# Optimization experiments

Hardware: AMD Instinct MI355X
Metric: run time of the kernel (lower is better)

Reference implementation:

```python
import jax, jax.numpy as jnp
import numpy as np

B, T = 256, 512          # sequences, timesteps (batched over pyro.markov loop)
DATA_DIM = 88            # piano-roll tones
HIDDEN_DIM = 16          # HMM latent states
NN_DIM = 48
NN_CHANNELS = 2
KERNEL = 3


def _uniform(key, shape, fan_in):
    bound = 1.0 / np.sqrt(fan_in)
    return jax.random.uniform(key, shape, minval=-bound, maxval=bound, dtype=jnp.float32)


def setup_inputs() -> dict:
    key = jax.random.key(0)
    ks = jax.random.split(key, 13)
    w = jax.random.randint(ks[0], (B, T, 1), 0, HIDDEN_DIM)
    x = jax.random.randint(ks[1], (B, T, 1), 0, HIDDEN_DIM)
    y = jax.random.uniform(ks[2], (B, T, DATA_DIM), dtype=jnp.float32)
    return {
        "w": w, "x": x, "y": y,
        # nn.Linear(hidden_dim, nn_dim) for x and w one-hots
        "W_xh": _uniform(ks[3], (NN_DIM, HIDDEN_DIM), HIDDEN_DIM),
        "b_xh": _uniform(ks[4], (NN_DIM,), HIDDEN_DIM),
        "W_wh": _uniform(ks[5], (NN_DIM, HIDDEN_DIM), HIDDEN_DIM),
        "b_wh": _uniform(ks[6], (NN_DIM,), HIDDEN_DIM),
        # nn.Linear(nn_channels*data_dim, nn_dim)
        "W_yh": _uniform(ks[7], (NN_DIM, NN_CHANNELS * DATA_DIM), NN_CHANNELS * DATA_DIM),
        "b_yh": _uniform(ks[8], (NN_DIM,), NN_CHANNELS * DATA_DIM),
        # nn.Conv1d(1, nn_channels, 3, padding=1)
        "W_conv": _uniform(ks[9], (NN_CHANNELS, 1, KERNEL), KERNEL),
        "b_conv": _uniform(ks[10], (NN_CHANNELS,), KERNEL),
        # nn.Linear(nn_dim, data_dim)
        "W_hl": _uniform(ks[11], (DATA_DIM, NN_DIM), NN_DIM),
        "b_hl": _uniform(ks[12], (DATA_DIM,), NN_DIM),
    }


def _tones_generator(w, x, y, W_xh, b_xh, W_wh, b_wh, W_yh, b_yh, W_conv, b_conv, W_hl, b_hl):
    b, t, d = y.shape
    # one-hot scatter of the latent state indices (trailing index dim of size 1)
    w_onehot = jax.nn.one_hot(w[..., 0], HIDDEN_DIM, dtype=y.dtype)   # [B,T,H]
    x_onehot = jax.nn.one_hot(x[..., 0], HIDDEN_DIM, dtype=y.dtype)   # [B,T,H]
    # Conv1d(1 -> nn_channels, k=3, pad=1) over the tone axis
    y_nch = y.reshape(b * t, 1, d)                                    # [BT,1,D]
    y_conv = jax.lax.conv_general_dilated(
        y_nch, W_conv, window_strides=(1,), padding=[(1, 1)],
        dimension_numbers=("NCH", "OIH", "NCH"))
    y_conv = jax.nn.relu(y_conv + b_conv[None, :, None])              # [BT,C,D]
    y_conv = y_conv.reshape(b, t, NN_CHANNELS * d)                    # [B,T,C*D]
    h = jax.nn.relu(
        jnp.einsum("bth,nh->btn", x_onehot, W_xh) + b_xh
        + jnp.einsum("bth,nh->btn", w_onehot, W_wh) + b_wh
        + jnp.einsum("btc,nc->btn", y_conv, W_yh) + b_yh)             # [B,T,ND]
    return jnp.einsum("btn,dn->btd", h, W_hl) + b_hl                  # [B,T,D]


def reference(w, x, y, W_xh, b_xh, W_wh, b_wh, W_yh, b_yh, W_conv, b_conv, W_hl, b_hl):
    return _tones_generator(w, x, y, W_xh, b_xh, W_wh, b_wh, W_yh, b_yh,
                            W_conv, b_conv, W_hl, b_hl)
```

## Files before the change

kernel.cpp:

```cpp
#include <hip/hip_runtime.h>
#include <stdint.h>

#define NTOK (256 * 512)
#define TPB 256

typedef short bf16x8 __attribute__((ext_vector_type(8)));
typedef float f32x4 __attribute__((ext_vector_type(4)));
typedef unsigned short u16;
typedef unsigned int u32;

#define B1_U16 10752
#define B2_U16 6144
#define W_BYTES ((B1_U16 + B2_U16) * 2)
#define W_CHUNKS (W_BYTES / 16)
#define YB_U16 2816
#define H_U16 1024

__device__ __forceinline__ u16 f2bf(float f) {
    u32 u = __float_as_uint(f);
    return (u16)((u + 0x7fffu + ((u >> 16) & 1u)) >> 16);
}
__device__ __forceinline__ u32 cvtpk(float lo, float hi) {
    u32 r;
    asm("v_cvt_pk_bf16_f32 %0, %1, %2" : "=v"(r) : "v"(lo), "v"(hi));
    return r;
}
__device__ __forceinline__ void gll16(const void* g, void* l) {
    __builtin_amdgcn_global_load_lds(
        (const __attribute__((address_space(1))) void*)g,
        (__attribute__((address_space(3))) void*)l, 16, 0, 0);
}
__device__ __forceinline__ void gll4(const void* g, void* l) {
    __builtin_amdgcn_global_load_lds(
        (const __attribute__((address_space(1))) void*)g,
        (__attribute__((address_space(3))) void*)l, 4, 0, 0);
}

__global__ __launch_bounds__(256, 1)
void prep_weights(const float* __restrict__ Wxh, const float* __restrict__ bxh,
                  const float* __restrict__ Wwh, const float* __restrict__ bwh,
                  const float* __restrict__ Wyh, const float* __restrict__ byh,
                  const float* __restrict__ Whl, const float* __restrict__ bhl,
                  u16* __restrict__ ws)
{
    int e = blockIdx.x * 256 + threadIdx.x;
    if (e < B1_U16) {
        int j = e & 7, n = (e >> 3) % 48, kc = e / 384;
        int k = kc * 8 + j;
        float v;
        if (k < 176)       v = Wyh[n * 176 + (k & 1) * 88 + (k >> 1)];
        else if (k < 192)  v = Wxh[n * 16 + (k - 176)];
        else if (k < 208)  v = Wwh[n * 16 + (k - 192)];
        else if (k == 208) v = bxh[n] + bwh[n] + byh[n];
        else               v = 0.0f;
        ws[e] = f2bf(v);
    } else if (e < B1_U16 + B2_U16) {
        int e2 = e - B1_U16;
        int j = e2 & 7, dd = (e2 >> 3) % 96, kc = e2 / 768;
        int k = kc * 8 + j;
        float v = 0.0f;
        if (dd < 88) {
            if (k < 48)       v = Whl[dd * 48 + k];
            else if (k == 48) v = bhl[dd];
        }
        ws[e] = f2bf(v);
    }
}

__global__ __launch_bounds__(256, 2)
void tones_v8(const int* __restrict__ widx, const int* __restrict__ xidx,
              const float* __restrict__ y,
              const float* __restrict__ Wconv, const float* __restrict__ bconv,
              const u16* __restrict__ wsb,
              float* __restrict__ out)
{
    __shared__ __align__(16) u16 lds[32256];

    const int tid = threadIdx.x;
    const int wave = tid >> 6, lane = tid & 63;
    const int q = lane >> 4, c = lane & 15;

    const int tb = blockIdx.x * 64 + wave * 16;

    #pragma unroll
    for (int i = 0; i < 8; i++) {
        const int cb = i * 256 + wave * 64;
        gll16((const char*)wsb + (cb + lane) * 16, (char*)lds + cb * 16);
    }
    if (wave == 0) {
        const int cb = 2048;
        gll16((const char*)wsb + (cb + lane) * 16, (char*)lds + cb * 16);
    }

    u16* sYu = lds + 16896 + wave * YB_U16;
    {
        const char* yt = (const char*)(y + (size_t)tb * 88);
        char* dst = (char*)sYu;
        #pragma unroll
        for (int j = 0; j < 5; j++)
            gll16(yt + j * 1024 + lane * 16, dst + j * 1024);
        #pragma unroll
        for (int k = 0; k < 2; k++)
            gll4(yt + 5120 + k * 256 + lane * 4, dst + 5120 + k * 256);
    }

    const int xv = xidx[tb + c];
    const int wv = widx[tb + c];
    const float wc00 = Wconv[0], wc01 = Wconv[1], wc02 = Wconv[2];
    const float wc10 = Wconv[3], wc11 = Wconv[4], wc12 = Wconv[5];
    const float bc0 = bconv[0], bc1 = bconv[1];

    u16* sW = lds + 28160 + wave * H_U16;
    if (lane < 32) {
        uint4 hz = make_uint4((lane < 16) ? 0x3F80u : 0u, 0, 0, 0);
        *(uint4*)(sW + ((6 + (lane >> 4)) * 16 + (lane & 15)) * 8) = hz;
    }

    __syncthreads();

    const float* yr = (const float*)sYu + c * 88;

    f32x4 h0 = {0, 0, 0, 0}, h1 = {0, 0, 0, 0}, h2 = {0, 0, 0, 0};

    const u16* f1 = lds + (q * 48 + c) * 8;
    const u16* f2 = lds + B1_U16 + (q * 96 + c) * 8;

    #pragma unroll
    for (int ks = 0; ks < 7; ks++) {
        bf16x8 af;
        if (ks < 5) {
            const int d0 = 16 * ks + 4 * q;
            float p0 = (d0 == 0) ? 0.0f : yr[d0 - 1];
            f32x4 v4 = *(const f32x4*)(yr + d0);
            float p5 = yr[d0 + 4];
            float p[6] = {p0, v4[0], v4[1], v4[2], v4[3], p5};
            #pragma unroll
            for (int i = 0; i < 4; i++) {
                float c0 = fmaf(wc00, p[i], fmaf(wc01, p[i + 1], fmaf(wc02, p[i + 2], bc0)));
                float c1 = fmaf(wc10, p[i], fmaf(wc11, p[i + 1], fmaf(wc12, p[i + 2], bc1)));
                u32 pk = cvtpk(fmaxf(c0, 0.0f), fmaxf(c1, 0.0f));
                af[2 * i]     = (short)(pk & 0xFFFF);
                af[2 * i + 1] = (short)(pk >> 16);
            }
        } else if (ks == 5) {
            if (q < 2) {
                const int d0 = 80 + 4 * q;
                float p0 = yr[d0 - 1];
                f32x4 v4 = *(const f32x4*)(yr + d0);
                float p5 = (q == 0) ? yr[84] : 0.0f;
                float p[6] = {p0, v4[0], v4[1], v4[2], v4[3], p5};
                #pragma unroll
                for (int i = 0; i < 4; i++) {
                    float c0 = fmaf(wc00, p[i], fmaf(wc01, p[i + 1], fmaf(wc02, p[i + 2], bc0)));
                    float c1 = fmaf(wc10, p[i], fmaf(wc11, p[i + 1], fmaf(wc12, p[i + 2], bc1)));
                    u32 pk = cvtpk(fmaxf(c0, 0.0f), fmaxf(c1, 0.0f));
                    af[2 * i]     = (short)(pk & 0xFFFF);
                    af[2 * i + 1] = (short)(pk >> 16);
                }
            } else {
                const int base = (q - 2) * 8;
                #pragma unroll
                for (int j = 0; j < 8; j++)
                    af[j] = (short)((base + j == xv) ? 0x3F80 : 0);
            }
        } else {
            if (q < 2) {
                const int base = q * 8;
                #pragma unroll
                for (int j = 0; j < 8; j++)
                    af[j] = (short)((base + j == wv) ? 0x3F80 : 0);
            } else {
                #pragma unroll
                for (int j = 0; j < 8; j++)
                    af[j] = (short)((q == 2 && j == 0) ? 0x3F80 : 0);
            }
        }
        bf16x8 b0 = *(const bf16x8*)(f1 + (ks * 192 +  0) * 8);
        bf16x8 b1 = *(const bf16x8*)(f1 + (ks * 192 + 16) * 8);
        bf16x8 b2 = *(const bf16x8*)(f1 + (ks * 192 + 32) * 8);
        h0 = __builtin_amdgcn_mfma_f32_16x16x32_bf16(af, b0, h0, 0, 0, 0);
        h1 = __builtin_amdgcn_mfma_f32_16x16x32_bf16(af, b1, h1, 0, 0, 0);
        h2 = __builtin_amdgcn_mfma_f32_16x16x32_bf16(af, b2, h2, 0, 0, 0);
    }

    #pragma unroll
    for (int r = 0; r < 4; r++) {
        const int row = q * 4 + r;
        sW[((0 + (c >> 3)) * 16 + row) * 8 + (c & 7)] = (u16)cvtpk(fmaxf(h0[r], 0.0f), 0.0f);
        sW[((2 + (c >> 3)) * 16 + row) * 8 + (c & 7)] = (u16)cvtpk(fmaxf(h1[r], 0.0f), 0.0f);
        sW[((4 + (c >> 3)) * 16 + row) * 8 + (c & 7)] = (u16)cvtpk(fmaxf(h2[r], 0.0f), 0.0f);
    }

    f32x4 o0 = {0,0,0,0}, o1 = {0,0,0,0}, o2 = {0,0,0,0};
    f32x4 o3 = {0,0,0,0}, o4 = {0,0,0,0}, o5 = {0,0,0,0};
    #pragma unroll
    for (int ks = 0; ks < 2; ks++) {
        bf16x8 a2 = *(const bf16x8*)(sW + ((ks * 4 + q) * 16 + c) * 8);
        bf16x8 w0 = *(const bf16x8*)(f2 + (ks * 384 +  0) * 8);
        bf16x8 w1 = *(const bf16x8*)(f2 + (ks * 384 + 16) * 8);
        bf16x8 w2 = *(const bf16x8*)(f2 + (ks * 384 + 32) * 8);
        bf16x8 w3 = *(const bf16x8*)(f2 + (ks * 384 + 48) * 8);
        bf16x8 w4 = *(const bf16x8*)(f2 + (ks * 384 + 64) * 8);
        bf16x8 w5 = *(const bf16x8*)(f2 + (ks * 384 + 80) * 8);
        o0 = __builtin_amdgcn_mfma_f32_16x16x32_bf16(a2, w0, o0, 0, 0, 0);
        o1 = __builtin_amdgcn_mfma_f32_16x16x32_bf16(a2, w1, o1, 0, 0, 0);
        o2 = __builtin_amdgcn_mfma_f32_16x16x32_bf16(a2, w2, o2, 0, 0, 0);
        o3 = __builtin_amdgcn_mfma_f32_16x16x32_bf16(a2, w3, o3, 0, 0, 0);
        o4 = __builtin_amdgcn_mfma_f32_16x16x32_bf16(a2, w4, o4, 0, 0, 0);
        o5 = __builtin_amdgcn_mfma_f32_16x16x32_bf16(a2, w5, o5, 0, 0, 0);
    }

    float* orow = out + (size_t)(tb + q * 4) * 88;
    #pragma unroll
    for (int r = 0; r < 4; r++) {
        orow[r * 88 +  0 + c] = o0[r];
        orow[r * 88 + 16 + c] = o1[r];
        orow[r * 88 + 32 + c] = o2[r];
        orow[r * 88 + 48 + c] = o3[r];
        orow[r * 88 + 64 + c] = o4[r];
        if (c < 8) orow[r * 88 + 80 + c] = o5[r];
    }
}

extern "C" void kernel_launch(void* const* d_in, const int* in_sizes, int n_in,
                              void* d_out, int out_size, void* d_ws, size_t ws_size,
                              hipStream_t stream) {
    (void)in_sizes; (void)n_in; (void)out_size; (void)ws_size;
    u16* ws = (u16*)d_ws;
    prep_weights<<<dim3(66), dim3(TPB), 0, stream>>>(
        (const float*)d_in[3],  (const float*)d_in[4],
        (const float*)d_in[5],  (const float*)d_in[6],
        (const float*)d_in[7],  (const float*)d_in[8],
        (const float*)d_in[11], (const float*)d_in[12], ws);
    tones_v8<<<dim3(NTOK / 64), dim3(TPB), 0, stream>>>(
        (const int*)d_in[0], (const int*)d_in[1], (const float*)d_in[2],
        (const float*)d_in[9], (const float*)d_in[10], ws, (float*)d_out);
}
```

Baseline: 124.7 us.

## Overlap weight staging with conv compute and stage output through LDS

Issues the per-tile y loads first and the weight LDS loads after them, split into contiguous per-wave chunks. A partial vmcnt wait lets each wave compute all conv and one-hot A fragments from its y tile while the weight loads are still in flight, replacing the block-wide syncthreads with a later wait plus barrier. Outputs are written to the wave's LDS y buffer and then stored to global memory as coalesced 16-byte vectors instead of scattered 4-byte stores. This raises register pressure by holding seven A fragments, and it depends on exact vmcnt counting being correct.

```diff
diff --git a/kernel.cpp b/kernel.cpp
--- a/kernel.cpp
+++ b/kernel.cpp
@@ -11,8 +11,6 @@
 
 #define B1_U16 10752
 #define B2_U16 6144
-#define W_BYTES ((B1_U16 + B2_U16) * 2)
-#define W_CHUNKS (W_BYTES / 16)
 #define YB_U16 2816
 #define H_U16 1024
 
@@ -68,7 +66,7 @@
 }
 
 __global__ __launch_bounds__(256, 2)
-void tones_v8(const int* __restrict__ widx, const int* __restrict__ xidx,
+void tones_v9(const int* __restrict__ widx, const int* __restrict__ xidx,
               const float* __restrict__ y,
               const float* __restrict__ Wconv, const float* __restrict__ bconv,
               const u16* __restrict__ wsb,
@@ -82,15 +80,8 @@
 
     const int tb = blockIdx.x * 64 + wave * 16;
 
-    #pragma unroll
-    for (int i = 0; i < 8; i++) {
-        const int cb = i * 256 + wave * 64;
-        gll16((const char*)wsb + (cb + lane) * 16, (char*)lds + cb * 16);
-    }
-    if (wave == 0) {
-        const int cb = 2048;
-        gll16((const char*)wsb + (cb + lane) * 16, (char*)lds + cb * 16);
-    }
+    const int xv = xidx[tb + c];
+    const int wv = widx[tb + c];
 
     u16* sYu = lds + 16896 + wave * YB_U16;
     {
@@ -104,8 +95,19 @@
             gll4(yt + 5120 + k * 256 + lane * 4, dst + 5120 + k * 256);
     }
 
-    const int xv = xidx[tb + c];
-    const int wv = widx[tb + c];
+    {
+        const int wb = wave * 528;
+        #pragma unroll
+        for (int i = 0; i < 8; i++) {
+            const int cb = wb + i * 64;
+            gll16((const char*)wsb + (cb + lane) * 16, (char*)lds + cb * 16);
+        }
+        if (lane < 16) {
+            const int cb = wb + 512;
+            gll16((const char*)wsb + (cb + lane) * 16, (char*)lds + cb * 16);
+        }
+    }
+
     const float wc00 = Wconv[0], wc01 = Wconv[1], wc02 = Wconv[2];
     const float wc10 = Wconv[3], wc11 = Wconv[4], wc12 = Wconv[5];
     const float bc0 = bconv[0], bc1 = bconv[1];
@@ -116,71 +118,79 @@
         *(uint4*)(sW + ((6 + (lane >> 4)) * 16 + (lane & 15)) * 8) = hz;
     }
 
-    __syncthreads();
+    asm volatile("s_waitcnt vmcnt(9)" ::: "memory");
+    __builtin_amdgcn_sched_barrier(0);
 
     const float* yr = (const float*)sYu + c * 88;
 
-    f32x4 h0 = {0, 0, 0, 0}, h1 = {0, 0, 0, 0}, h2 = {0, 0, 0, 0};
-
-    const u16* f1 = lds + (q * 48 + c) * 8;
-    const u16* f2 = lds + B1_U16 + (q * 96 + c) * 8;
-
-    #pragma unroll
-    for (int ks = 0; ks < 7; ks++) {
-        bf16x8 af;
-        if (ks < 5) {
-            const int d0 = 16 * ks + 4 * q;
-            float p0 = (d0 == 0) ? 0.0f : yr[d0 - 1];
+    bf16x8 afr[7];
+    #pragma unroll
+    for (int ks = 0; ks < 5; ks++) {
+        const int d0 = 16 * ks + 4 * q;
+        float p0 = (d0 == 0) ? 0.0f : yr[d0 - 1];
+        f32x4 v4 = *(const f32x4*)(yr + d0);
+        float p5 = yr[d0 + 4];
+        float p[6] = {p0, v4[0], v4[1], v4[2], v4[3], p5};
+        #pragma unroll
+        for (int i = 0; i < 4; i++) {
+            float c0 = fmaf(wc00, p[i], fmaf(wc01, p[i + 1], fmaf(wc02, p[i + 2], bc0)));
+            float c1 = fmaf(wc10, p[i], fmaf(wc11, p[i + 1], fmaf(wc12, p[i + 2], bc1)));
+            u32 pk = cvtpk(fmaxf(c0, 0.0f), fmaxf(c1, 0.0f));
+            afr[ks][2 * i]     = (short)(pk & 0xFFFF);
+            afr[ks][2 * i + 1] = (short)(pk >> 16);
+        }
+    }
+    {
+        if (q < 2) {
+            const int d0 = 80 + 4 * q;
+            float p0 = yr[d0 - 1];
             f32x4 v4 = *(const f32x4*)(yr + d0);
-            float p5 = yr[d0 + 4];
+            float p5 = (q == 0) ? yr[84] : 0.0f;
             float p[6] = {p0, v4[0], v4[1], v4[2], v4[3], p5};
             #pragma unroll
             for (int i = 0; i < 4; i++) {
                 float c0 = fmaf(wc00, p[i], fmaf(wc01, p[i + 1], fmaf(wc02, p[i + 2], bc0)));
                 float c1 = fmaf(wc10, p[i], fmaf(wc11, p[i + 1], fmaf(wc12, p[i + 2], bc1)));
                 u32 pk = cvtpk(fmaxf(c0, 0.0f), fmaxf(c1, 0.0f));
-                af[2 * i]     = (short)(pk & 0xFFFF);
-                af[2 * i + 1] = (short)(pk >> 16);
-            }
-        } else if (ks == 5) {
-            if (q < 2) {
-                const int d0 = 80 + 4 * q;
-                float p0 = yr[d0 - 1];
-                f32x4 v4 = *(const f32x4*)(yr + d0);
-                float p5 = (q == 0) ? yr[84] : 0.0f;
-                float p[6] = {p0, v4[0], v4[1], v4[2], v4[3], p5};
-                #pragma unroll
-                for (int i = 0; i < 4; i++) {
-                    float c0 = fmaf(wc00, p[i], fmaf(wc01, p[i + 1], fmaf(wc02, p[i + 2], bc0)));
-                    float c1 = fmaf(wc10, p[i], fmaf(wc11, p[i + 1], fmaf(wc12, p[i + 2], bc1)));
-                    u32 pk = cvtpk(fmaxf(c0, 0.0f), fmaxf(c1, 0.0f));
-                    af[2 * i]     = (short)(pk & 0xFFFF);
-                    af[2 * i + 1] = (short)(pk >> 16);
-                }
-            } else {
-                const int base = (q - 2) * 8;
-                #pragma unroll
-                for (int j = 0; j < 8; j++)
-                    af[j] = (short)((base + j == xv) ? 0x3F80 : 0);
+                afr[5][2 * i]     = (short)(pk & 0xFFFF);
+                afr[5][2 * i + 1] = (short)(pk >> 16);
             }
         } else {
-            if (q < 2) {
-                const int base = q * 8;
-                #pragma unroll
-                for (int j = 0; j < 8; j++)
-                    af[j] = (short)((base + j == wv) ? 0x3F80 : 0);
-            } else {
-                #pragma unroll
-                for (int j = 0; j < 8; j++)
-                    af[j] = (short)((q == 2 && j == 0) ? 0x3F80 : 0);
-            }
-        }
+            const int base = (q - 2) * 8;
+            #pragma unroll
+            for (int j = 0; j < 8; j++)
+                afr[5][j] = (short)((base + j == xv) ? 0x3F80 : 0);
+        }
+    }
+    {
+        if (q < 2) {
+            const int base = q * 8;
+            #pragma unroll
+            for (int j = 0; j < 8; j++)
+                afr[6][j] = (short)((base + j == wv) ? 0x3F80 : 0);
+        } else {
+            #pragma unroll
+            for (int j = 0; j < 8; j++)
+                afr[6][j] = (short)((q == 2 && j == 0) ? 0x3F80 : 0);
+        }
+    }
+
+    __builtin_amdgcn_sched_barrier(0);
+    asm volatile("s_waitcnt vmcnt(0)" ::: "memory");
+    __builtin_amdgcn_s_barrier();
+
+    const u16* f1 = lds + (q * 48 + c) * 8;
+    const u16* f2 = lds + B1_U16 + (q * 96 + c) * 8;
+
+    f32x4 h0 = {0, 0, 0, 0}, h1 = {0, 0, 0, 0}, h2 = {0, 0, 0, 0};
+    #pragma unroll
+    for (int ks = 0; ks < 7; ks++) {
         bf16x8 b0 = *(const bf16x8*)(f1 + (ks * 192 +  0) * 8);
         bf16x8 b1 = *(const bf16x8*)(f1 + (ks * 192 + 16) * 8);
         bf16x8 b2 = *(const bf16x8*)(f1 + (ks * 192 + 32) * 8);
-        h0 = __builtin_amdgcn_mfma_f32_16x16x32_bf16(af, b0, h0, 0, 0, 0);
-        h1 = __builtin_amdgcn_mfma_f32_16x16x32_bf16(af, b1, h1, 0, 0, 0);
-        h2 = __builtin_amdgcn_mfma_f32_16x16x32_bf16(af, b2, h2, 0, 0, 0);
+        h0 = __builtin_amdgcn_mfma_f32_16x16x32_bf16(afr[ks], b0, h0, 0, 0, 0);
+        h1 = __builtin_amdgcn_mfma_f32_16x16x32_bf16(afr[ks], b1, h1, 0, 0, 0);
+        h2 = __builtin_amdgcn_mfma_f32_16x16x32_bf16(afr[ks], b2, h2, 0, 0, 0);
     }
 
     #pragma unroll
@@ -210,15 +220,25 @@
         o5 = __builtin_amdgcn_mfma_f32_16x16x32_bf16(a2, w5, o5, 0, 0, 0);
     }
 
-    float* orow = out + (size_t)(tb + q * 4) * 88;
+    float* sO = (float*)sYu;
     #pragma unroll
     for (int r = 0; r < 4; r++) {
-        orow[r * 88 +  0 + c] = o0[r];
-        orow[r * 88 + 16 + c] = o1[r];
-        orow[r * 88 + 32 + c] = o2[r];
-        orow[r * 88 + 48 + c] = o3[r];
-        orow[r * 88 + 64 + c] = o4[r];
-        if (c < 8) orow[r * 88 + 80 + c] = o5[r];
+        const int row = q * 4 + r;
+        sO[row * 88 +  0 + c] = o0[r];
+        sO[row * 88 + 16 + c] = o1[r];
+        sO[row * 88 + 32 + c] = o2[r];
+        sO[row * 88 + 48 + c] = o3[r];
+        sO[row * 88 + 64 + c] = o4[r];
+        if (c < 8) sO[row * 88 + 80 + c] = o5[r];
+    }
+    {
+        const f32x4* sOv = (const f32x4*)sYu;
+        f32x4* og = (f32x4*)(out + (size_t)tb * 88);
+        #pragma unroll
+        for (int j = 0; j < 5; j++)
+            og[j * 64 + lane] = sOv[j * 64 + lane];
+        if (lane < 32)
+            og[320 + lane] = sOv[320 + lane];
     }
 }
 
@@ -232,7 +252,7 @@
         (const float*)d_in[5],  (const float*)d_in[6],
         (const float*)d_in[7],  (const float*)d_in[8],
         (const float*)d_in[11], (const float*)d_in[12], ws);
-    tones_v8<<<dim3(NTOK / 64), dim3(TPB), 0, stream>>>(
+    tones_v9<<<dim3(NTOK / 64), dim3(TPB), 0, stream>>>(
         (const int*)d_in[0], (const int*)d_in[1], (const float*)d_in[2],
         (const float*)d_in[9], (const float*)d_in[10], ws, (float*)d_out);
 }
```

Result: slower. 127.9 us (+2.6%).

## Process four token tiles per wave with double-buffered y staging

Applied to the files above, without the earlier changes.

Each block now handles 256 tokens instead of 64, with each wave looping over four 16-token tiles. The shared weight staging is amortized across more tokens, and y tiles are prefetched into a second LDS buffer while the current tile computes. The hidden scratch reuses the y buffer, which cuts LDS use. This relies on hand-written vmcnt waits that are fragile with interleaved global stores, and the grid is smaller, which reduces parallelism.

```diff
diff --git a/kernel.cpp b/kernel.cpp
--- a/kernel.cpp
+++ b/kernel.cpp
@@ -11,10 +11,8 @@
 
 #define B1_U16 10752
 #define B2_U16 6144
-#define W_BYTES ((B1_U16 + B2_U16) * 2)
-#define W_CHUNKS (W_BYTES / 16)
+#define W_U16 (B1_U16 + B2_U16)
 #define YB_U16 2816
-#define H_U16 1024
 
 __device__ __forceinline__ u16 f2bf(float f) {
     u32 u = __float_as_uint(f);
@@ -34,6 +32,17 @@
     __builtin_amdgcn_global_load_lds(
         (const __attribute__((address_space(1))) void*)g,
         (__attribute__((address_space(3))) void*)l, 4, 0, 0);
+}
+
+__device__ __forceinline__ void stage_y(const float* ysrc, u16* dst_u16, int lane) {
+    const char* yt = (const char*)ysrc;
+    char* dst = (char*)dst_u16;
+    #pragma unroll
+    for (int j = 0; j < 5; j++)
+        gll16(yt + j * 1024 + lane * 16, dst + j * 1024);
+    #pragma unroll
+    for (int k = 0; k < 2; k++)
+        gll4(yt + 5120 + k * 256 + lane * 4, dst + 5120 + k * 256);
 }
 
 __global__ __launch_bounds__(256, 1)
@@ -67,64 +76,18 @@
     }
 }
 
-__global__ __launch_bounds__(256, 2)
-void tones_v8(const int* __restrict__ widx, const int* __restrict__ xidx,
-              const float* __restrict__ y,
-              const float* __restrict__ Wconv, const float* __restrict__ bconv,
-              const u16* __restrict__ wsb,
-              float* __restrict__ out)
+__device__ __forceinline__ void compute_tile(
+    const u16* __restrict__ ldsw,
+    u16* __restrict__ sb,
+    float wc00, float wc01, float wc02, float wc10, float wc11, float wc12,
+    float bc0, float bc1, int xv, int wv, int q, int c, int tb,
+    float* __restrict__ out)
 {
-    __shared__ __align__(16) u16 lds[32256];
-
-    const int tid = threadIdx.x;
-    const int wave = tid >> 6, lane = tid & 63;
-    const int q = lane >> 4, c = lane & 15;
-
-    const int tb = blockIdx.x * 64 + wave * 16;
-
-    #pragma unroll
-    for (int i = 0; i < 8; i++) {
-        const int cb = i * 256 + wave * 64;
-        gll16((const char*)wsb + (cb + lane) * 16, (char*)lds + cb * 16);
-    }
-    if (wave == 0) {
-        const int cb = 2048;
-        gll16((const char*)wsb + (cb + lane) * 16, (char*)lds + cb * 16);
-    }
-
-    u16* sYu = lds + 16896 + wave * YB_U16;
-    {
-        const char* yt = (const char*)(y + (size_t)tb * 88);
-        char* dst = (char*)sYu;
-        #pragma unroll
-        for (int j = 0; j < 5; j++)
-            gll16(yt + j * 1024 + lane * 16, dst + j * 1024);
-        #pragma unroll
-        for (int k = 0; k < 2; k++)
-            gll4(yt + 5120 + k * 256 + lane * 4, dst + 5120 + k * 256);
-    }
-
-    const int xv = xidx[tb + c];
-    const int wv = widx[tb + c];
-    const float wc00 = Wconv[0], wc01 = Wconv[1], wc02 = Wconv[2];
-    const float wc10 = Wconv[3], wc11 = Wconv[4], wc12 = Wconv[5];
-    const float bc0 = bconv[0], bc1 = bconv[1];
-
-    u16* sW = lds + 28160 + wave * H_U16;
-    if (lane < 32) {
-        uint4 hz = make_uint4((lane < 16) ? 0x3F80u : 0u, 0, 0, 0);
-        *(uint4*)(sW + ((6 + (lane >> 4)) * 16 + (lane & 15)) * 8) = hz;
-    }
-
-    __syncthreads();
-
-    const float* yr = (const float*)sYu + c * 88;
+    const float* yr = (const float*)sb + c * 88;
+    const u16* f1 = ldsw + (q * 48 + c) * 8;
+    const u16* f2 = ldsw + B1_U16 + (q * 96 + c) * 8;
 
     f32x4 h0 = {0, 0, 0, 0}, h1 = {0, 0, 0, 0}, h2 = {0, 0, 0, 0};
-
-    const u16* f1 = lds + (q * 48 + c) * 8;
-    const u16* f2 = lds + B1_U16 + (q * 96 + c) * 8;
-
     #pragma unroll
     for (int ks = 0; ks < 7; ks++) {
         bf16x8 af;
@@ -183,6 +146,11 @@
         h2 = __builtin_amdgcn_mfma_f32_16x16x32_bf16(af, b2, h2, 0, 0, 0);
     }
 
+    u16* sW = sb;
+    if (q < 2) {
+        uint4 hz = make_uint4((q == 0) ? 0x3F80u : 0u, 0, 0, 0);
+        *(uint4*)(sW + ((6 + q) * 16 + c) * 8) = hz;
+    }
     #pragma unroll
     for (int r = 0; r < 4; r++) {
         const int row = q * 4 + r;
@@ -222,6 +190,63 @@
     }
 }
 
+__global__ __launch_bounds__(256, 2)
+void tones_v10(const int* __restrict__ widx, const int* __restrict__ xidx,
+               const float* __restrict__ y,
+               const float* __restrict__ Wconv, const float* __restrict__ bconv,
+               const u16* __restrict__ wsb,
+               float* __restrict__ out)
+{
+    __shared__ __align__(16) u16 lds[16896 + 4 * 2 * YB_U16];
+
+    const int tid = threadIdx.x;
+    const int wave = tid >> 6, lane = tid & 63;
+    const int q = lane >> 4, c = lane & 15;
+    const int base = blockIdx.x * 256 + wave * 64;
+
+    int xv[4], wv[4];
+    #pragma unroll
+    for (int t = 0; t < 4; t++) {
+        xv[t] = xidx[base + t * 16 + c];
+        wv[t] = widx[base + t * 16 + c];
+    }
+
+    u16* buf0 = lds + W_U16 + wave * (2 * YB_U16);
+    u16* buf1 = buf0 + YB_U16;
+
+    stage_y(y + (size_t)base * 88, buf0, lane);
+
+    {
+        const int wb = wave * 528;
+        #pragma unroll
+        for (int i = 0; i < 8; i++) {
+            const int cb = wb + i * 64;
+            gll16((const char*)wsb + (cb + lane) * 16, (char*)lds + cb * 16);
+        }
+        if (lane < 16) {
+            const int cb = wb + 512;
+            gll16((const char*)wsb + (cb + lane) * 16, (char*)lds + cb * 16);
+        }
+    }
+
+    stage_y(y + (size_t)(base + 16) * 88, buf1, lane);
+
+    const float wc00 = Wconv[0], wc01 = Wconv[1], wc02 = Wconv[2];
+    const float wc10 = Wconv[3], wc11 = Wconv[4], wc12 = Wconv[5];
+    const float bc0 = bconv[0], bc1 = bconv[1];
+
+    #pragma unroll
+    for (int t = 0; t < 4; t++) {
+        u16* sb = (t & 1) ? buf1 : buf0;
+        if (t >= 1 && t < 3)
+            stage_y(y + (size_t)(base + (t + 1) * 16) * 88, (t & 1) ? buf0 : buf1, lane);
+        asm volatile("s_waitcnt vmcnt(7)" ::: "memory");
+        if (t == 0) __builtin_amdgcn_s_barrier();
+        compute_tile(lds, sb, wc00, wc01, wc02, wc10, wc11, wc12, bc0, bc1,
+                     xv[t], wv[t], q, c, base + t * 16, out);
+    }
+}
+
 extern "C" void kernel_launch(void* const* d_in, const int* in_sizes, int n_in,
                               void* d_out, int out_size, void* d_ws, size_t ws_size,
                               hipStream_t stream) {
@@ -232,7 +257,7 @@
         (const float*)d_in[5],  (const float*)d_in[6],
         (const float*)d_in[7],  (const float*)d_in[8],
         (const float*)d_in[11], (const float*)d_in[12], ws);
-    tones_v8<<<dim3(NTOK / 64), dim3(TPB), 0, stream>>>(
+    tones_v10<<<dim3(NTOK / 256), dim3(TPB), 0, stream>>>(
         (const int*)d_in[0], (const int*)d_in[1], (const float*)d_in[2],
         (const float*)d_in[9], (const float*)d_in[10], ws, (float*)d_out);
 }
```

After: 126.0 us. Within noise of the previous version (+1.0%).

## Double tokens per block and pass hidden activations via bpermute instead of LDS

Applied to the files above, without the earlier changes.

The block grows to 512 threads covering 128 tokens, so the bf16 weight staging in LDS is amortized over twice as many tokens, and the weight load is split evenly across 8 waves. The first MFMA swaps its operands so the hidden result comes out transposed. The hidden activations are then packed and redistributed with ds_bpermute into the second GEMM's A fragment, replacing the per-wave LDS scratch round trip. One-hot fragment construction is also written as packed 32-bit words. The larger block and LDS footprint may lower occupancy per CU.

```diff
diff --git a/kernel.cpp b/kernel.cpp
--- a/kernel.cpp
+++ b/kernel.cpp
@@ -2,19 +2,19 @@
 #include <stdint.h>
 
 #define NTOK (256 * 512)
-#define TPB 256
 
 typedef short bf16x8 __attribute__((ext_vector_type(8)));
 typedef float f32x4 __attribute__((ext_vector_type(4)));
+typedef unsigned int u32x4 __attribute__((ext_vector_type(4)));
 typedef unsigned short u16;
 typedef unsigned int u32;
 
+union Frag { bf16x8 h; u32x4 w; };
+
 #define B1_U16 10752
 #define B2_U16 6144
-#define W_BYTES ((B1_U16 + B2_U16) * 2)
-#define W_CHUNKS (W_BYTES / 16)
+#define W_U16 (B1_U16 + B2_U16)
 #define YB_U16 2816
-#define H_U16 1024
 
 __device__ __forceinline__ u16 f2bf(float f) {
     u32 u = __float_as_uint(f);
@@ -67,32 +67,25 @@
     }
 }
 
-__global__ __launch_bounds__(256, 2)
-void tones_v8(const int* __restrict__ widx, const int* __restrict__ xidx,
-              const float* __restrict__ y,
-              const float* __restrict__ Wconv, const float* __restrict__ bconv,
-              const u16* __restrict__ wsb,
-              float* __restrict__ out)
+__global__ __launch_bounds__(512, 4)
+void tones_v12(const int* __restrict__ widx, const int* __restrict__ xidx,
+               const float* __restrict__ y,
+               const float* __restrict__ Wconv, const float* __restrict__ bconv,
+               const u16* __restrict__ wsb,
+               float* __restrict__ out)
 {
-    __shared__ __align__(16) u16 lds[32256];
+    __shared__ __align__(16) u16 lds[W_U16 + 8 * YB_U16];
 
     const int tid = threadIdx.x;
     const int wave = tid >> 6, lane = tid & 63;
     const int q = lane >> 4, c = lane & 15;
 
-    const int tb = blockIdx.x * 64 + wave * 16;
-
-    #pragma unroll
-    for (int i = 0; i < 8; i++) {
-        const int cb = i * 256 + wave * 64;
-        gll16((const char*)wsb + (cb + lane) * 16, (char*)lds + cb * 16);
-    }
-    if (wave == 0) {
-        const int cb = 2048;
-        gll16((const char*)wsb + (cb + lane) * 16, (char*)lds + cb * 16);
-    }
-
-    u16* sYu = lds + 16896 + wave * YB_U16;
+    const int tb = blockIdx.x * 128 + wave * 16;
+
+    const int xv = xidx[tb + c];
+    const int wv = widx[tb + c];
+
+    u16* sYu = lds + W_U16 + wave * YB_U16;
     {
         const char* yt = (const char*)(y + (size_t)tb * 88);
         char* dst = (char*)sYu;
@@ -104,30 +97,34 @@
             gll4(yt + 5120 + k * 256 + lane * 4, dst + 5120 + k * 256);
     }
 
-    const int xv = xidx[tb + c];
-    const int wv = widx[tb + c];
+    {
+        const int wb = wave * 264;
+        #pragma unroll
+        for (int i = 0; i < 4; i++) {
+            const int cb = wb + i * 64;
+            gll16((const char*)wsb + (cb + lane) * 16, (char*)lds + cb * 16);
+        }
+        if (lane < 8) {
+            const int cb = wb + 256;
+            gll16((const char*)wsb + (cb + lane) * 16, (char*)lds + cb * 16);
+        }
+    }
+
     const float wc00 = Wconv[0], wc01 = Wconv[1], wc02 = Wconv[2];
     const float wc10 = Wconv[3], wc11 = Wconv[4], wc12 = Wconv[5];
     const float bc0 = bconv[0], bc1 = bconv[1];
 
-    u16* sW = lds + 28160 + wave * H_U16;
-    if (lane < 32) {
-        uint4 hz = make_uint4((lane < 16) ? 0x3F80u : 0u, 0, 0, 0);
-        *(uint4*)(sW + ((6 + (lane >> 4)) * 16 + (lane & 15)) * 8) = hz;
-    }
-
     __syncthreads();
 
     const float* yr = (const float*)sYu + c * 88;
-
-    f32x4 h0 = {0, 0, 0, 0}, h1 = {0, 0, 0, 0}, h2 = {0, 0, 0, 0};
 
     const u16* f1 = lds + (q * 48 + c) * 8;
     const u16* f2 = lds + B1_U16 + (q * 96 + c) * 8;
 
+    f32x4 h0 = {0, 0, 0, 0}, h1 = {0, 0, 0, 0}, h2 = {0, 0, 0, 0};
     #pragma unroll
     for (int ks = 0; ks < 7; ks++) {
-        bf16x8 af;
+        Frag af;
         if (ks < 5) {
             const int d0 = 16 * ks + 4 * q;
             float p0 = (d0 == 0) ? 0.0f : yr[d0 - 1];
@@ -138,9 +135,7 @@
             for (int i = 0; i < 4; i++) {
                 float c0 = fmaf(wc00, p[i], fmaf(wc01, p[i + 1], fmaf(wc02, p[i + 2], bc0)));
                 float c1 = fmaf(wc10, p[i], fmaf(wc11, p[i + 1], fmaf(wc12, p[i + 2], bc1)));
-                u32 pk = cvtpk(fmaxf(c0, 0.0f), fmaxf(c1, 0.0f));
-                af[2 * i]     = (short)(pk & 0xFFFF);
-                af[2 * i + 1] = (short)(pk >> 16);
+                af.w[i] = cvtpk(fmaxf(c0, 0.0f), fmaxf(c1, 0.0f));
             }
         } else if (ks == 5) {
             if (q < 2) {
@@ -153,49 +148,76 @@
                 for (int i = 0; i < 4; i++) {
                     float c0 = fmaf(wc00, p[i], fmaf(wc01, p[i + 1], fmaf(wc02, p[i + 2], bc0)));
                     float c1 = fmaf(wc10, p[i], fmaf(wc11, p[i + 1], fmaf(wc12, p[i + 2], bc1)));
-                    u32 pk = cvtpk(fmaxf(c0, 0.0f), fmaxf(c1, 0.0f));
-                    af[2 * i]     = (short)(pk & 0xFFFF);
-                    af[2 * i + 1] = (short)(pk >> 16);
+                    af.w[i] = cvtpk(fmaxf(c0, 0.0f), fmaxf(c1, 0.0f));
                 }
             } else {
                 const int base = (q - 2) * 8;
                 #pragma unroll
-                for (int j = 0; j < 8; j++)
-                    af[j] = (short)((base + j == xv) ? 0x3F80 : 0);
+                for (int i = 0; i < 4; i++) {
+                    u32 lo = (base + 2 * i     == xv) ? 0x3F80u : 0u;
+                    u32 hi = (base + 2 * i + 1 == xv) ? 0x3F800000u : 0u;
+                    af.w[i] = lo | hi;
+                }
             }
         } else {
             if (q < 2) {
                 const int base = q * 8;
                 #pragma unroll
-                for (int j = 0; j < 8; j++)
-                    af[j] = (short)((base + j == wv) ? 0x3F80 : 0);
+                for (int i = 0; i < 4; i++) {
+                    u32 lo = (base + 2 * i     == wv) ? 0x3F80u : 0u;
+                    u32 hi = (base + 2 * i + 1 == wv) ? 0x3F800000u : 0u;
+                    af.w[i] = lo | hi;
+                }
             } else {
-                #pragma unroll
-                for (int j = 0; j < 8; j++)
-                    af[j] = (short)((q == 2 && j == 0) ? 0x3F80 : 0);
+                af.w = (u32x4){(q == 2) ? 0x3F80u : 0u, 0u, 0u, 0u};
             }
         }
         bf16x8 b0 = *(const bf16x8*)(f1 + (ks * 192 +  0) * 8);
         bf16x8 b1 = *(const bf16x8*)(f1 + (ks * 192 + 16) * 8);
         bf16x8 b2 = *(const bf16x8*)(f1 + (ks * 192 + 32) * 8);
-        h0 = __builtin_amdgcn_mfma_f32_16x16x32_bf16(af, b0, h0, 0, 0, 0);
-        h1 = __builtin_amdgcn_mfma_f32_16x16x32_bf16(af, b1, h1, 0, 0, 0);
-        h2 = __builtin_amdgcn_mfma_f32_16x16x32_bf16(af, b2, h2, 0, 0, 0);
-    }
-
-    #pragma unroll
-    for (int r = 0; r < 4; r++) {
-        const int row = q * 4 + r;
-        sW[((0 + (c >> 3)) * 16 + row) * 8 + (c & 7)] = (u16)cvtpk(fmaxf(h0[r], 0.0f), 0.0f);
-        sW[((2 + (c >> 3)) * 16 + row) * 8 + (c & 7)] = (u16)cvtpk(fmaxf(h1[r], 0.0f), 0.0f);
-        sW[((4 + (c >> 3)) * 16 + row) * 8 + (c & 7)] = (u16)cvtpk(fmaxf(h2[r], 0.0f), 0.0f);
-    }
+        h0 = __builtin_amdgcn_mfma_f32_16x16x32_bf16(b0, af.h, h0, 0, 0, 0);
+        h1 = __builtin_amdgcn_mfma_f32_16x16x32_bf16(b1, af.h, h1, 0, 0, 0);
+        h2 = __builtin_amdgcn_mfma_f32_16x16x32_bf16(b2, af.h, h2, 0, 0, 0);
+    }
+
+    u32 pk00 = cvtpk(fmaxf(h0[0], 0.0f), fmaxf(h0[1], 0.0f));
+    u32 pk01 = cvtpk(fmaxf(h0[2], 0.0f), fmaxf(h0[3], 0.0f));
+    u32 pk10 = cvtpk(fmaxf(h1[0], 0.0f), fmaxf(h1[1], 0.0f));
+    u32 pk11 = cvtpk(fmaxf(h1[2], 0.0f), fmaxf(h1[3], 0.0f));
+    u32 pk20 = cvtpk(fmaxf(h2[0], 0.0f), fmaxf(h2[1], 0.0f));
+    u32 pk21 = cvtpk(fmaxf(h2[2], 0.0f), fmaxf(h2[3], 0.0f));
+
+    const int a0 = ((((2 * q) & 3) * 16 + c) * 4);
+    const int a1 = a0 + 64;
+    u32 A00 = (u32)__builtin_amdgcn_ds_bpermute(a0, (int)pk00);
+    u32 A01 = (u32)__builtin_amdgcn_ds_bpermute(a0, (int)pk01);
+    u32 B00 = (u32)__builtin_amdgcn_ds_bpermute(a1, (int)pk00);
+    u32 B01 = (u32)__builtin_amdgcn_ds_bpermute(a1, (int)pk01);
+    u32 A10 = (u32)__builtin_amdgcn_ds_bpermute(a0, (int)pk10);
+    u32 A11 = (u32)__builtin_amdgcn_ds_bpermute(a0, (int)pk11);
+    u32 B10 = (u32)__builtin_amdgcn_ds_bpermute(a1, (int)pk10);
+    u32 B11 = (u32)__builtin_amdgcn_ds_bpermute(a1, (int)pk11);
+    u32 A20 = (u32)__builtin_amdgcn_ds_bpermute(a0, (int)pk20);
+    u32 A21 = (u32)__builtin_amdgcn_ds_bpermute(a0, (int)pk21);
+    u32 B20 = (u32)__builtin_amdgcn_ds_bpermute(a1, (int)pk20);
+    u32 B21 = (u32)__builtin_amdgcn_ds_bpermute(a1, (int)pk21);
+
+    const bool hi = (q >= 2);
+    Frag a2k0, a2k1;
+    a2k0.w[0] = hi ? A10 : A00;
+    a2k0.w[1] = hi ? A11 : A01;
+    a2k0.w[2] = hi ? B10 : B00;
+    a2k0.w[3] = hi ? B11 : B01;
+    a2k1.w[0] = !hi ? A20 : ((q == 2) ? 0x3F80u : 0u);
+    a2k1.w[1] = !hi ? A21 : 0u;
+    a2k1.w[2] = !hi ? B20 : 0u;
+    a2k1.w[3] = !hi ? B21 : 0u;
 
     f32x4 o0 = {0,0,0,0}, o1 = {0,0,0,0}, o2 = {0,0,0,0};
     f32x4 o3 = {0,0,0,0}, o4 = {0,0,0,0}, o5 = {0,0,0,0};
     #pragma unroll
     for (int ks = 0; ks < 2; ks++) {
-        bf16x8 a2 = *(const bf16x8*)(sW + ((ks * 4 + q) * 16 + c) * 8);
+        bf16x8 a2 = (ks == 0) ? a2k0.h : a2k1.h;
         bf16x8 w0 = *(const bf16x8*)(f2 + (ks * 384 +  0) * 8);
         bf16x8 w1 = *(const bf16x8*)(f2 + (ks * 384 + 16) * 8);
         bf16x8 w2 = *(const bf16x8*)(f2 + (ks * 384 + 32) * 8);
@@ -227,12 +249,12 @@
                               hipStream_t stream) {
     (void)in_sizes; (void)n_in; (void)out_size; (void)ws_size;
     u16* ws = (u16*)d_ws;
-    prep_weights<<<dim3(66), dim3(TPB), 0, stream>>>(
+    prep_weights<<<dim3(66), dim3(256), 0, stream>>>(
         (const float*)d_in[3],  (const float*)d_in[4],
         (const float*)d_in[5],  (const float*)d_in[6],
         (const float*)d_in[7],  (const float*)d_in[8],
         (const float*)d_in[11], (const float*)d_in[12], ws);
-    tones_v8<<<dim3(NTOK / 64), dim3(TPB), 0, stream>>>(
+    tones_v12<<<dim3(NTOK / 128), dim3(512), 0, stream>>>(
         (const int*)d_in[0], (const int*)d_in[1], (const float*)d_in[2],
         (const float*)d_in[9], (const float*)d_in[10], ws, (float*)d_out);
 }
```

Measured after the change: 123.8 us. About the same (-0.8%).
